# Kernel optimization log

Measured on AMD Instinct MI355X. Metric: run time of the kernel, lower is better.

The kernel has to match this reference:

```python
import jax, jax.numpy as jnp
import numpy as np

B, DM, H, W = 2, 96, 48, 48
E = 192          # d_expand == d_inner
R, N = 6, 16     # delta_rank, d_state


def conv2d(x, w, b, groups=1, pad=0):
    out = jax.lax.conv_general_dilated(
        x, w, window_strides=(1, 1), padding=[(pad, pad), (pad, pad)],
        dimension_numbers=("NCHW", "OIHW", "NCHW"), feature_group_count=groups)
    return out + b[None, :, None, None]


def setup_inputs() -> dict:
    key = jax.random.key(0)
    ks = jax.random.split(key, 24)
    f = lambda k, shape, s: jax.random.normal(k, shape, jnp.float32) * s
    inp = {
        "x": jax.random.normal(ks[0], (B, DM, H, W), jnp.float32),
        "in_proj_w": f(ks[1], (2 * E, DM), 0.05),
        "conv_w": f(ks[2], (E, 1, 3, 3), 0.2),
        "conv_b": f(ks[3], (E,), 0.1),
        "x_proj_w": f(ks[4], (4, R + 2 * N, E), 0.01),
        "dt_proj_w": f(ks[5], (4, E, R), 0.01),
        "dt_proj_b": jnp.full((4, E), -9.0) + f(ks[6], (4, E), 0.1),
        "A_log": jnp.tile(jnp.log(jnp.arange(1, N + 1, dtype=jnp.float32))[None, None, :], (4, E, 1)),
        "Ds": jnp.ones((4, E), jnp.float32),
        "ln_g": jnp.ones(E, jnp.float32), "ln_b": jnp.zeros(E, jnp.float32),
        "c1_w": f(ks[7], (2 * E, E, 1, 1), 0.05), "c1_b": jnp.zeros(2 * E),
        "bn1_g": jnp.ones(2 * E), "bn1_b": jnp.zeros(2 * E), "bn1_m": jnp.zeros(2 * E), "bn1_v": jnp.ones(2 * E),
        "c2_w": f(ks[8], (2 * E, 1, 3, 3), 0.2), "c2_b": jnp.zeros(2 * E),
        "bn2_g": jnp.ones(2 * E), "bn2_b": jnp.zeros(2 * E), "bn2_m": jnp.zeros(2 * E), "bn2_v": jnp.ones(2 * E),
        "c3_w": f(ks[9], (E // 2, 2 * E, 1, 1), 0.05), "c3_b": jnp.zeros(E // 2),
        "se1_w": f(ks[10], (E // 4, E // 2), 0.1), "se1_b": jnp.zeros(E // 4),
        "se2_w": f(ks[11], (E // 2, E // 4), 0.1), "se2_b": jnp.zeros(E // 2),
    }
    return inp


def reference(x, in_proj_w, conv_w, conv_b, x_proj_w, dt_proj_w, dt_proj_b,
              A_log, Ds, ln_g, ln_b,
              c1_w, c1_b, bn1_g, bn1_b, bn1_m, bn1_v,
              c2_w, c2_b, bn2_g, bn2_b, bn2_m, bn2_v,
              c3_w, c3_b, se1_w, se1_b, se2_w, se2_b):
    Bs, _, Hs, Ws = x.shape
    L = Hs * Ws
    # in projection (Linear over channel dim), split x/z gates
    xz = jnp.einsum("bchw,oc->bohw", x, in_proj_w)
    xi, z = jnp.split(xz, 2, axis=1)
    # depthwise conv + SiLU
    xi = jax.nn.silu(conv2d(xi, conv_w, conv_b, groups=E, pad=1))
    # ---- selective scan (4-direction cross scan, cumsum formulation) ----
    xf = xi.reshape(Bs, E, L)
    xt = jnp.swapaxes(xi, 2, 3).reshape(Bs, E, L)
    xs = jnp.stack([xf, xf[..., ::-1], xt, xt[..., ::-1]], axis=1)  # [B,4,E,L]
    dbc = jnp.einsum("bkcl,krc->bkrl", xs, x_proj_w)                # [B,4,R+2N,L]
    dlt, b, c = dbc[:, :, :R], dbc[:, :, R:R + N], dbc[:, :, R + N:]
    dlt = jnp.einsum("bkrl,kdr->bkdl", dlt, dt_proj_w) + dt_proj_b[None, :, :, None]
    dlt = jax.nn.softplus(dlt)                                      # [B,4,E,L]
    dA = dlt[..., None] * A_log[None, :, :, None, :]                # [B,4,E,L,N]
    phi = jnp.exp(-jnp.cumsum(dA, axis=3))
    dbx = dlt[..., None] * jnp.swapaxes(b, 2, 3)[:, :, None] * xs[..., None]  # [B,4,E,L,N]
    h = phi * jnp.cumsum(dbx / (phi + 1e-12), axis=3)
    y = jnp.einsum("bkdln,bknl->bkdl", h, c) + Ds[None, :, :, None]  # [B,4,E,L]
    # ---- cross merge ----
    y1 = y[:, 0]
    y2 = y[:, 1, :, ::-1]
    y3 = jnp.swapaxes(y[:, 2].reshape(Bs, E, Ws, Hs), 2, 3).reshape(Bs, E, L)
    y4 = jnp.swapaxes(y[:, 3, :, ::-1].reshape(Bs, E, Ws, Hs), 2, 3).reshape(Bs, E, L)
    ys = (y1 + y2 + y3 + y4).reshape(Bs, E, Hs, Ws)
    # layernorm over channels
    yn = jnp.moveaxis(ys, 1, -1)
    mu = yn.mean(-1, keepdims=True)
    var = yn.var(-1, keepdims=True)
    yn = (yn - mu) / jnp.sqrt(var + 1e-5) * ln_g + ln_b
    u = jnp.moveaxis(yn, -1, 1) * z
    # ---- EFFN ----
    def bn(t, g, bb, m, v):
        return (t - m[None, :, None, None]) / jnp.sqrt(v + 1e-5)[None, :, None, None] * g[None, :, None, None] + bb[None, :, None, None]
    t = jax.nn.relu(bn(conv2d(u, c1_w, c1_b), bn1_g, bn1_b, bn1_m, bn1_v))
    t = jax.nn.relu(bn(conv2d(t, c2_w, c2_b, groups=2 * E, pad=1), bn2_g, bn2_b, bn2_m, bn2_v))
    t = conv2d(t, c3_w, c3_b)
    # squeeze-excitation: t + t * sigmoid(fc(relu(fc(avgpool(t)))))
    s = t.mean((2, 3))
    s = jax.nn.relu(s @ se1_w.T + se1_b)
    s = jax.nn.sigmoid(s @ se2_w.T + se2_b)
    return t + t * s[:, :, None, None]
```

## Files before the change

kernel.cpp:

```cpp
#include <hip/hip_runtime.h>
#include <hip/hip_bf16.h>

#define LTOT 2304
#define ECH  192
#define NCH  16
#define CCH  96
#define SCH  24

__device__ __forceinline__ int permS(int k, int l) {
  if (k == 0) return l;
  if (k == 1) return LTOT - 1 - l;
  int m = (k == 2) ? l : (LTOT - 1 - l);
  return (m % 48) * 48 + (m / 48);
}

__device__ __forceinline__ float sp_fast(float x) {
  float t = __expf(x);
  return (t <= 0.018f) ? t * fmaf(t, fmaf(t, 0.33333334f, -0.5f), 1.f) : log1pf(t);
}

__global__ __launch_bounds__(256) void k1_inproj(const float* __restrict__ x,
                                                 const float* __restrict__ W,
                                                 float* __restrict__ xi_pre,
                                                 float* __restrict__ z) {
  const int l0 = blockIdx.x * 64;
  const int o0 = blockIdx.y * 64;
  const int b  = blockIdx.z;
  __shared__ __align__(16) float xs[96 * 66];
  __shared__ __align__(16) float Wl[96 * 68];
  const int tid = threadIdx.x;
  for (int idx = tid; idx < 96 * 64; idx += 256) {
    int i = idx & 63, cc = idx >> 6;
    xs[cc * 66 + i] = x[(b * 96 + cc) * LTOT + l0 + i];
  }
  for (int idx = tid; idx < 64 * 96; idx += 256) {
    int r = idx / 96, cc = idx - r * 96;
    Wl[cc * 68 + r] = W[(o0 + r) * 96 + cc];
  }
  __syncthreads();
  const int lane = tid & 63, w = tid >> 6;
  const int jj = lane & 15, rqq = lane >> 4;
  const int rbase = 16 * w + 4 * rqq;
  float acc[4][4];
#pragma unroll
  for (int p = 0; p < 4; ++p)
#pragma unroll
    for (int t = 0; t < 4; ++t) acc[p][t] = 0.f;
#pragma unroll 2
  for (int cc = 0; cc < 96; ++cc) {
    const float4 wv = *(const float4*)&Wl[cc * 68 + rbase];
    const float2 xa = *(const float2*)&xs[cc * 66 + 2 * jj];
    const float2 xb = *(const float2*)&xs[cc * 66 + 32 + 2 * jj];
    acc[0][0] = fmaf(wv.x, xa.x, acc[0][0]); acc[0][1] = fmaf(wv.y, xa.x, acc[0][1]);
    acc[0][2] = fmaf(wv.z, xa.x, acc[0][2]); acc[0][3] = fmaf(wv.w, xa.x, acc[0][3]);
    acc[1][0] = fmaf(wv.x, xa.y, acc[1][0]); acc[1][1] = fmaf(wv.y, xa.y, acc[1][1]);
    acc[1][2] = fmaf(wv.z, xa.y, acc[1][2]); acc[1][3] = fmaf(wv.w, xa.y, acc[1][3]);
    acc[2][0] = fmaf(wv.x, xb.x, acc[2][0]); acc[2][1] = fmaf(wv.y, xb.x, acc[2][1]);
    acc[2][2] = fmaf(wv.z, xb.x, acc[2][2]); acc[2][3] = fmaf(wv.w, xb.x, acc[2][3]);
    acc[3][0] = fmaf(wv.x, xb.y, acc[3][0]); acc[3][1] = fmaf(wv.y, xb.y, acc[3][1]);
    acc[3][2] = fmaf(wv.z, xb.y, acc[3][2]); acc[3][3] = fmaf(wv.w, xb.y, acc[3][3]);
  }
  __syncthreads();
  float* ol = xs;
#pragma unroll
  for (int t = 0; t < 4; ++t) {
    ol[(rbase + t) * 65 + 2 * jj]      = acc[0][t];
    ol[(rbase + t) * 65 + 2 * jj + 1]  = acc[1][t];
    ol[(rbase + t) * 65 + 2 * jj + 32] = acc[2][t];
    ol[(rbase + t) * 65 + 2 * jj + 33] = acc[3][t];
  }
  __syncthreads();
  for (int idx = tid; idx < 64 * 64; idx += 256) {
    int r = idx & 63, pos = idx >> 6;
    float v = ol[r * 65 + pos];
    int o = o0 + r, l = l0 + pos;
    if (o < ECH) xi_pre[(b * LTOT + l) * ECH + o] = v;
    else         z[(b * LTOT + l) * ECH + (o - ECH)] = v;
  }
}

__global__ __launch_bounds__(256) void k2_dwconv(const float* __restrict__ xi_pre,
                                                 const float* __restrict__ cw,
                                                 const float* __restrict__ cb,
                                                 float* __restrict__ xi) {
  int g = blockIdx.x * 256 + threadIdx.x;
  if (g >= 2 * LTOT * ECH) return;
  int e = g % ECH; int l = (g / ECH) % LTOT; int b = g / (ECH * LTOT);
  int h = l / 48, wq = l % 48;
  float acc = cb[e];
#pragma unroll
  for (int kh = 0; kh < 3; ++kh) {
    int hh = h + kh - 1; if (hh < 0 || hh >= 48) continue;
#pragma unroll
    for (int kw = 0; kw < 3; ++kw) {
      int ww = wq + kw - 1; if (ww < 0 || ww >= 48) continue;
      acc = fmaf(cw[e * 9 + kh * 3 + kw], xi_pre[(b * LTOT + hh * 48 + ww) * ECH + e], acc);
    }
  }
  xi[g] = acc / (1.f + __expf(-acc));
}

__global__ __launch_bounds__(256) void k3_xproj(const float* __restrict__ xi,
                                                const float* __restrict__ xw,
                                                float* __restrict__ dl6g,
                                                float* __restrict__ bT,
                                                float* __restrict__ cT) {
  const int l0 = blockIdx.x * 32;
  const int k  = blockIdx.y;
  const int b  = blockIdx.z;
  __shared__ __align__(16) float xs[96 * 34];
  __shared__ __align__(16) float Wl[192 * 40];
  __shared__ float dl6[6 * 33];
  const int tid = threadIdx.x;
  const float* wsrc = xw + k * 38 * ECH;
  for (int idx = tid; idx < 38 * 192; idx += 256) {
    int r = idx / 192, cc = idx - r * 192;
    Wl[cc * 40 + r] = wsrc[idx];
  }
  const int lane = tid & 63, w = tid >> 6;
  const int jj = lane & 15;
  const int rq = w * 4 + (lane >> 4);
  const int rqc = rq < 9 ? rq : 9;
  const int j0 = 2 * jj;
  float a00 = 0.f, a01 = 0.f, a02 = 0.f, a03 = 0.f;
  float a10 = 0.f, a11 = 0.f, a12 = 0.f, a13 = 0.f;
  for (int kc = 0; kc < 2; ++kc) {
    __syncthreads();
    for (int idx = tid; idx < 32 * 96; idx += 256) {
      int j = idx / 96, cc = idx - j * 96;
      int s = permS(k, l0 + j);
      xs[cc * 34 + j] = xi[(b * LTOT + s) * ECH + kc * 96 + cc];
    }
    __syncthreads();
#pragma unroll 4
    for (int cc = 0; cc < 96; ++cc) {
      const float2 xv = *(const float2*)&xs[cc * 34 + j0];
      const float4 wv = *(const float4*)&Wl[(kc * 96 + cc) * 40 + 4 * rqc];
      a00 = fmaf(wv.x, xv.x, a00); a01 = fmaf(wv.y, xv.x, a01);
      a02 = fmaf(wv.z, xv.x, a02); a03 = fmaf(wv.w, xv.x, a03);
      a10 = fmaf(wv.x, xv.y, a10); a11 = fmaf(wv.y, xv.y, a11);
      a12 = fmaf(wv.z, xv.y, a12); a13 = fmaf(wv.w, xv.y, a13);
    }
  }
  const int bk = b * 4 + k;
  if (rq < 10) {
    float av[2][4] = {{a00, a01, a02, a03}, {a10, a11, a12, a13}};
#pragma unroll
    for (int t = 0; t < 4; ++t) {
      int r = 4 * rq + t;
      if (r >= 38) continue;
#pragma unroll
      for (int p = 0; p < 2; ++p) {
        int j = j0 + p;
        float v = av[p][t];
        if (r < 6)       dl6g[((bk * LTOT) + l0 + j) * 6 + r] = v;
        else if (r < 22) bT[((bk * LTOT) + l0 + j) * NCH + (r - 6)] = v;
        else             cT[((bk * LTOT) + l0 + j) * NCH + (r - 22)] = v;
      }
    }
  }
}

__global__ __launch_bounds__(256) void k4a_scan1(const float* __restrict__ dl6g,
                                                 const float* __restrict__ xi,
                                                 const float* __restrict__ bT,
                                                 const float* __restrict__ Alog,
                                                 const float* __restrict__ dtw,
                                                 const float* __restrict__ dtb,
                                                 float* __restrict__ q,
                                                 float* __restrict__ Ts) {
  const int cb = blockIdx.x;
  const int db = blockIdx.y;
  const int bk = blockIdx.z;
  const int b = bk >> 2, k = bk & 3;
  const int l0 = cb * 96;
  __shared__ __align__(16) float2 sdx[48 * 64];
  __shared__ __align__(16) float  sb[96 * NCH];
  __shared__ __align__(16) float  sdl6[96 * 6];
  const int tid = threadIdx.x;
  const int dd = tid & 63, cg = tid >> 6;
  const int dg = db * 64 + dd;
  float b6 = dtb[k * ECH + dg];
  float w6[6];
  {
    const float2* d2 = (const float2*)(dtw + (k * ECH + dg) * 6);
    float2 u0 = d2[0], u1 = d2[1], u2 = d2[2];
    w6[0] = u0.x; w6[1] = u0.y; w6[2] = u1.x; w6[3] = u1.y; w6[4] = u2.x; w6[5] = u2.y;
  }
  for (int idx = tid; idx < 96 * 6; idx += 256) sdl6[idx] = dl6g[(bk * LTOT + l0) * 6 + idx];
  for (int idx = tid; idx < 96 * NCH; idx += 256) sb[idx] = bT[(bk * LTOT + l0) * NCH + idx];
  float C1[16], h[16];
#pragma unroll
  for (int n = 0; n < 16; ++n) {
    C1[n] = Alog[(k * ECH + dg) * NCH + n];
    h[n] = 0.f;
  }
  float Tsum = 0.f;
  const int c = cb * 4 + cg;
  for (int half = 0; half < 2; ++half) {
    __syncthreads();
    for (int e = tid; e < 48 * 64; e += 256) {
      int s = e >> 6;
      int j = (s / 12) * 24 + half * 12 + (s % 12);
      const float* d6 = sdl6 + j * 6;
      float xa = b6;
#pragma unroll
      for (int r = 0; r < 6; ++r) xa = fmaf(w6[r], d6[r], xa);
      float dl = sp_fast(xa);
      int sp = permS(k, l0 + j);
      float xiv = xi[(b * LTOT + sp) * ECH + dg];
      sdx[s * 64 + dd] = make_float2(dl, xiv);
    }
    __syncthreads();
    for (int i = 0; i < 12; ++i) {
      int j = cg * 24 + half * 12 + i;
      float2 dx = sdx[(cg * 12 + i) * 64 + dd];
      float dl = dx.x;
      float u  = dl * dx.y;
      Tsum += dl;
      const float4* bb4 = (const float4*)(sb + j * NCH);
      float4 q0 = bb4[0], q1 = bb4[1], q2 = bb4[2], q3 = bb4[3];
      float bbl[16] = {q0.x, q0.y, q0.z, q0.w, q1.x, q1.y, q1.z, q1.w,
                       q2.x, q2.y, q2.z, q2.w, q3.x, q3.y, q3.z, q3.w};
      if (dl <= 0.018f) {
#pragma unroll
        for (int n = 0; n < 16; ++n) {
          float xn = C1[n] * dl;
          float e = fmaf(xn, fmaf(xn, fmaf(xn, -(1.f / 6.f), 0.5f), -1.f), 1.f);
          h[n] = fmaf(e, h[n], u * bbl[n]);
        }
      } else {
#pragma unroll
        for (int n = 0; n < 16; ++n) {
          float e = __expf(-C1[n] * dl);
          h[n] = fmaf(e, h[n], u * bbl[n]);
        }
      }
    }
  }
  float4* qp = (float4*)(q + ((bk * CCH + c) * ECH + dg) * NCH);
  qp[0] = make_float4(h[0], h[1], h[2], h[3]);
  qp[1] = make_float4(h[4], h[5], h[6], h[7]);
  qp[2] = make_float4(h[8], h[9], h[10], h[11]);
  qp[3] = make_float4(h[12], h[13], h[14], h[15]);
  Ts[(bk * CCH + c) * ECH + dg] = Tsum;
}

__global__ __launch_bounds__(256) void k4b_comb(const float* __restrict__ Alog,
                                                const float* __restrict__ Ts,
                                                float* __restrict__ q) {
  int t = blockIdx.x * 256 + threadIdx.x;
  if (t >= 8 * ECH * NCH) return;
  int n = t & 15, d = (t >> 4) % ECH, bk = t / (NCH * ECH);
  int k = bk & 3;
  float A = Alog[(k * ECH + d) * NCH + n];
  float h = 0.f;
  for (int c = 0; c < CCH; ++c) {
    int base = ((bk * CCH + c) * ECH + d) * NCH + n;
    float qc = q[base];
    q[base] = h;
    float xv = A * Ts[(bk * CCH + c) * ECH + d];
    float P = (xv <= 0.05f)
                  ? fmaf(xv, fmaf(xv, fmaf(xv, -(1.f / 6.f), 0.5f), -1.f), 1.f)
                  : __expf(-xv);
    h = fmaf(P, h, qc);
  }
}

__global__ __launch_bounds__(256) void k4c_scan2(const float* __restrict__ dl6g,
                                                 const float* __restrict__ xi,
                                                 const float* __restrict__ bT,
                                                 const float* __restrict__ cT,
                                                 const float* __restrict__ Alog,
                                                 const float* __restrict__ dtw,
                                                 const float* __restrict__ dtb,
                                                 const float* __restrict__ hin,
                                                 float* __restrict__ yd) {
  const int cb = blockIdx.x;
  const int db = blockIdx.y;
  const int bk = blockIdx.z;
  const int b = bk >> 2, k = bk & 3;
  const int l0 = cb * 96;
  __shared__ __align__(16) float2 sdx[48 * 64];
  __shared__ __align__(16) float  sb[96 * NCH];
  __shared__ __align__(16) float  sc[96 * NCH];
  __shared__ __align__(16) float  sdl6[96 * 6];
  const int tid = threadIdx.x;
  const int dd = tid & 63, cg = tid >> 6;
  const int dg = db * 64 + dd;
  float b6 = dtb[k * ECH + dg];
  float w6[6];
  {
    const float2* d2 = (const float2*)(dtw + (k * ECH + dg) * 6);
    float2 u0 = d2[0], u1 = d2[1], u2 = d2[2];
    w6[0] = u0.x; w6[1] = u0.y; w6[2] = u1.x; w6[3] = u1.y; w6[4] = u2.x; w6[5] = u2.y;
  }
  for (int idx = tid; idx < 96 * 6; idx += 256) sdl6[idx] = dl6g[(bk * LTOT + l0) * 6 + idx];
  for (int idx = tid; idx < 96 * NCH; idx += 256) {
    sb[idx] = bT[(bk * LTOT + l0) * NCH + idx];
    sc[idx] = cT[(bk * LTOT + l0) * NCH + idx];
  }
  float C1[16], h[16];
  const int c = cb * 4 + cg;
  const float4* hp = (const float4*)(hin + ((bk * CCH + c) * ECH + dg) * NCH);
  {
    float4 h0 = hp[0], h1 = hp[1], h2 = hp[2], h3 = hp[3];
    h[0]=h0.x; h[1]=h0.y; h[2]=h0.z; h[3]=h0.w;
    h[4]=h1.x; h[5]=h1.y; h[6]=h1.z; h[7]=h1.w;
    h[8]=h2.x; h[9]=h2.y; h[10]=h2.z; h[11]=h2.w;
    h[12]=h3.x; h[13]=h3.y; h[14]=h3.z; h[15]=h3.w;
  }
#pragma unroll
  for (int n = 0; n < 16; ++n) C1[n] = Alog[(k * ECH + dg) * NCH + n];
  float* ydk = yd + (b * 4 + k) * LTOT * ECH;
  for (int half = 0; half < 2; ++half) {
    __syncthreads();
    for (int e = tid; e < 48 * 64; e += 256) {
      int s = e >> 6;
      int j = (s / 12) * 24 + half * 12 + (s % 12);
      const float* d6 = sdl6 + j * 6;
      float xa = b6;
#pragma unroll
      for (int r = 0; r < 6; ++r) xa = fmaf(w6[r], d6[r], xa);
      float dl = sp_fast(xa);
      int sp = permS(k, l0 + j);
      float xiv = xi[(b * LTOT + sp) * ECH + dg];
      sdx[s * 64 + dd] = make_float2(dl, xiv);
    }
    __syncthreads();
    for (int i = 0; i < 12; ++i) {
      int j = cg * 24 + half * 12 + i;
      float2 dx = sdx[(cg * 12 + i) * 64 + dd];
      float dl = dx.x;
      float u  = dl * dx.y;
      const float4* bb4 = (const float4*)(sb + j * NCH);
      float4 q0 = bb4[0], q1 = bb4[1], q2 = bb4[2], q3 = bb4[3];
      float bbl[16] = {q0.x, q0.y, q0.z, q0.w, q1.x, q1.y, q1.z, q1.w,
                       q2.x, q2.y, q2.z, q2.w, q3.x, q3.y, q3.z, q3.w};
      if (dl <= 0.018f) {
#pragma unroll
        for (int n = 0; n < 16; ++n) {
          float xn = C1[n] * dl;
          float e = fmaf(xn, fmaf(xn, fmaf(xn, -(1.f / 6.f), 0.5f), -1.f), 1.f);
          h[n] = fmaf(e, h[n], u * bbl[n]);
        }
      } else {
#pragma unroll
        for (int n = 0; n < 16; ++n) {
          float e = __expf(-C1[n] * dl);
          h[n] = fmaf(e, h[n], u * bbl[n]);
        }
      }
      const float4* cc4 = (const float4*)(sc + j * NCH);
      float4 c0 = cc4[0], c1 = cc4[1], c2 = cc4[2], c3 = cc4[3];
      float ccl[16] = {c0.x, c0.y, c0.z, c0.w, c1.x, c1.y, c1.z, c1.w,
                       c2.x, c2.y, c2.z, c2.w, c3.x, c3.y, c3.z, c3.w};
      float y = 0.f;
#pragma unroll
      for (int n = 0; n < 16; ++n) y = fmaf(h[n], ccl[n], y);
      int sp = permS(k, l0 + j);
      ydk[sp * ECH + dg] = y;
    }
  }
}

__global__ __launch_bounds__(256) void k5_ln(const float* __restrict__ yd,
                                             const float* __restrict__ Ds,
                                             const float* __restrict__ lng,
                                             const float* __restrict__ lnb,
                                             float* __restrict__ zu) {
  int p = blockIdx.x * 4 + (threadIdx.x >> 6);
  int lane = threadIdx.x & 63;
  int b = (p >= LTOT) ? 1 : 0;
  int l = p - b * LTOT;
  const float* y0 = yd + (b * 4) * LTOT * ECH + l * ECH;
  float vd[3], sd[3];
#pragma unroll
  for (int t = 0; t < 3; ++t) {
    int d = lane + t * 64;
    vd[t] = ((y0[d] + y0[LTOT * ECH + d]) + y0[2 * LTOT * ECH + d]) + y0[3 * LTOT * ECH + d];
    sd[t] = Ds[d] + Ds[ECH + d] + Ds[2 * ECH + d] + Ds[3 * ECH + d];
  }
  float s1 = vd[0] + vd[1] + vd[2];
  float s2 = sd[0] + sd[1] + sd[2];
#pragma unroll
  for (int off = 32; off > 0; off >>= 1) {
    s1 += __shfl_xor(s1, off, 64);
    s2 += __shfl_xor(s2, off, 64);
  }
  float mean_dot = s1 * (1.f / 192.f);
  float mean_sd  = s2 * (1.f / 192.f);
  float dev[3];
  float ss = 0.f;
#pragma unroll
  for (int t = 0; t < 3; ++t) {
    dev[t] = (vd[t] - mean_dot) + (sd[t] - mean_sd);
    ss = fmaf(dev[t], dev[t], ss);
  }
#pragma unroll
  for (int off = 32; off > 0; off >>= 1) ss += __shfl_xor(ss, off, 64);
  float rstd = 1.f / sqrtf(ss * (1.f / 192.f) + 1e-5f);
#pragma unroll
  for (int t = 0; t < 3; ++t) {
    int d = lane + t * 64;
    float yn = (dev[t] * rstd) * lng[d] + lnb[d];
    zu[p * ECH + d] = yn * zu[p * ECH + d];
  }
}

__global__ __launch_bounds__(256) void k6_c1(const float* __restrict__ u,
                                             const float* __restrict__ W,
                                             const float* __restrict__ c1b,
                                             const float* __restrict__ g1,
                                             const float* __restrict__ b1,
                                             const float* __restrict__ m1,
                                             const float* __restrict__ v1,
                                             float* __restrict__ t1,
                                             float* __restrict__ se) {
  const int l0 = blockIdx.x * 64;
  const int o0 = blockIdx.y * 64;
  const int b  = blockIdx.z;
  const int tid = threadIdx.x;
  if (blockIdx.x == 0 && blockIdx.y == 0 && blockIdx.z == 0 && tid < 192) se[tid] = 0.f;
  __shared__ __align__(16) float xs[96 * 66];
  __shared__ __align__(16) float Wl[96 * 68];
  const int lane = tid & 63, w = tid >> 6;
  const int jj = lane & 15, rqq = lane >> 4;
  const int rbase = 16 * w + 4 * rqq;
  float acc[4][4];
#pragma unroll
  for (int p = 0; p < 4; ++p)
#pragma unroll
    for (int t = 0; t < 4; ++t) acc[p][t] = 0.f;
  for (int kc = 0; kc < 2; ++kc) {
    if (kc) __syncthreads();
    for (int idx = tid; idx < 64 * 96; idx += 256) {
      int i = idx / 96, cc = idx - i * 96;
      xs[cc * 66 + i] = u[(b * LTOT + l0 + i) * ECH + kc * 96 + cc];
    }
    for (int idx = tid; idx < 64 * 96; idx += 256) {
      int r = idx / 96, cc = idx - r * 96;
      Wl[cc * 68 + r] = W[(o0 + r) * ECH + kc * 96 + cc];
    }
    __syncthreads();
#pragma unroll 2
    for (int cc = 0; cc < 96; ++cc) {
      const float4 wv = *(const float4*)&Wl[cc * 68 + rbase];
      const float2 xa = *(const float2*)&xs[cc * 66 + 2 * jj];
      const float2 xb = *(const float2*)&xs[cc * 66 + 32 + 2 * jj];
      acc[0][0] = fmaf(wv.x, xa.x, acc[0][0]); acc[0][1] = fmaf(wv.y, xa.x, acc[0][1]);
      acc[0][2] = fmaf(wv.z, xa.x, acc[0][2]); acc[0][3] = fmaf(wv.w, xa.x, acc[0][3]);
      acc[1][0] = fmaf(wv.x, xa.y, acc[1][0]); acc[1][1] = fmaf(wv.y, xa.y, acc[1][1]);
      acc[1][2] = fmaf(wv.z, xa.y, acc[1][2]); acc[1][3] = fmaf(wv.w, xa.y, acc[1][3]);
      acc[2][0] = fmaf(wv.x, xb.x, acc[2][0]); acc[2][1] = fmaf(wv.y, xb.x, acc[2][1]);
      acc[2][2] = fmaf(wv.z, xb.x, acc[2][2]); acc[2][3] = fmaf(wv.w, xb.x, acc[2][3]);
      acc[3][0] = fmaf(wv.x, xb.y, acc[3][0]); acc[3][1] = fmaf(wv.y, xb.y, acc[3][1]);
      acc[3][2] = fmaf(wv.z, xb.y, acc[3][2]); acc[3][3] = fmaf(wv.w, xb.y, acc[3][3]);
    }
  }
#pragma unroll
  for (int t = 0; t < 4; ++t) {
    int o = o0 + rbase + t;
    float sc = g1[o] / sqrtf(v1[o] + 1e-5f);
    float bias = (c1b[o] - m1[o]) * sc + b1[o];
#pragma unroll
    for (int p = 0; p < 4; ++p) acc[p][t] = fmaxf(fmaf(acc[p][t], sc, bias), 0.f);
  }
  __syncthreads();
  float* ol = xs;
#pragma unroll
  for (int t = 0; t < 4; ++t) {
    ol[(rbase + t) * 65 + 2 * jj]      = acc[0][t];
    ol[(rbase + t) * 65 + 2 * jj + 1]  = acc[1][t];
    ol[(rbase + t) * 65 + 2 * jj + 32] = acc[2][t];
    ol[(rbase + t) * 65 + 2 * jj + 33] = acc[3][t];
  }
  __syncthreads();
  for (int idx = tid; idx < 64 * 64; idx += 256) {
    int pos = idx & 63, r = idx >> 6;
    t1[(b * 384 + o0 + r) * LTOT + l0 + pos] = ol[r * 65 + pos];
  }
}

__global__ __launch_bounds__(256) void k7_dw2(const float* __restrict__ t1,
                                              const float* __restrict__ cw,
                                              const float* __restrict__ cb,
                                              const float* __restrict__ g2,
                                              const float* __restrict__ b2,
                                              const float* __restrict__ m2,
                                              const float* __restrict__ v2,
                                              float* __restrict__ t2) {
  int g = blockIdx.x * 256 + threadIdx.x;
  if (g >= 2 * LTOT * 384) return;
  int l = g % LTOT; int o = (g / LTOT) % 384; int b = g / (LTOT * 384);
  int h = l / 48, wq = l % 48;
  const float* src = t1 + (b * 384 + o) * LTOT;
  float acc = cb[o];
#pragma unroll
  for (int kh = 0; kh < 3; ++kh) {
    int hh = h + kh - 1; if (hh < 0 || hh >= 48) continue;
#pragma unroll
    for (int kw = 0; kw < 3; ++kw) {
      int ww = wq + kw - 1; if (ww < 0 || ww >= 48) continue;
      acc = fmaf(cw[o * 9 + kh * 3 + kw], src[hh * 48 + ww], acc);
    }
  }
  float sc = g2[o] / sqrtf(v2[o] + 1e-5f);
  float val = (acc - m2[o]) * sc + b2[o];
  t2[g] = fmaxf(val, 0.f);
}

__global__ __launch_bounds__(256) void k8_c3(const float* __restrict__ t2,
                                             const float* __restrict__ W,
                                             const float* __restrict__ c3b,
                                             float* __restrict__ t3,
                                             float* __restrict__ se) {
  const int l0 = blockIdx.x * 32;
  const int r0 = blockIdx.y * 32;
  const int b  = blockIdx.z;
  __shared__ __align__(16) float Wl[384 * 34];
  __shared__ __align__(16) float xs[192 * 34];
  const int tid = threadIdx.x;
  const int lane = tid & 63, w = tid >> 6;
  const int jj = lane & 15, rqq = lane >> 4;
  const int rloc = 8 * w + 2 * rqq;
  for (int idx = tid; idx < 32 * 384; idx += 256) {
    int r = idx / 384, cc = idx - r * 384;
    Wl[cc * 34 + r] = W[(r0 + r) * 384 + cc];
  }
  float acc[2][2];
  acc[0][0] = acc[0][1] = acc[1][0] = acc[1][1] = 0.f;
  for (int kc = 0; kc < 2; ++kc) {
    if (kc) __syncthreads();
    for (int idx = tid; idx < 192 * 32; idx += 256) {
      int i = idx & 31, cc = idx >> 5;
      xs[cc * 34 + i] = t2[(b * 384 + kc * 192 + cc) * LTOT + l0 + i];
    }
    __syncthreads();
#pragma unroll 4
    for (int cc = 0; cc < 192; ++cc) {
      const float2 wv = *(const float2*)&Wl[(kc * 192 + cc) * 34 + rloc];
      const float2 xv = *(const float2*)&xs[cc * 34 + 2 * jj];
      acc[0][0] = fmaf(wv.x, xv.x, acc[0][0]); acc[0][1] = fmaf(wv.y, xv.x, acc[0][1]);
      acc[1][0] = fmaf(wv.x, xv.y, acc[1][0]); acc[1][1] = fmaf(wv.y, xv.y, acc[1][1]);
    }
  }
  {
    float b0 = c3b[r0 + rloc], b1v = c3b[r0 + rloc + 1];
    acc[0][0] += b0; acc[1][0] += b0; acc[0][1] += b1v; acc[1][1] += b1v;
  }
#pragma unroll
  for (int t = 0; t < 2; ++t) {
    float v = acc[0][t] + acc[1][t];
    v += __shfl_xor(v, 1); v += __shfl_xor(v, 2);
    v += __shfl_xor(v, 4); v += __shfl_xor(v, 8);
    if (jj == 0) atomicAdd(&se[b * 96 + r0 + rloc + t], v);
  }
  __syncthreads();
  float* ol = xs;
#pragma unroll
  for (int t = 0; t < 2; ++t) {
    ol[(rloc + t) * 33 + 2 * jj]     = acc[0][t];
    ol[(rloc + t) * 33 + 2 * jj + 1] = acc[1][t];
  }
  __syncthreads();
  for (int idx = tid; idx < 32 * 32; idx += 256) {
    int pos = idx & 31, r = idx >> 5;
    t3[(b * 96 + r0 + r) * LTOT + l0 + pos] = ol[r * 33 + pos];
  }
}

__global__ __launch_bounds__(256) void k9a_se(const float* __restrict__ se,
                                              const float* __restrict__ w1,
                                              const float* __restrict__ sb1,
                                              const float* __restrict__ w2,
                                              const float* __restrict__ sb2,
                                              float* __restrict__ smul) {
  __shared__ float sm[192];
  __shared__ float s1[96];
  int t = threadIdx.x;
  if (t < 192) sm[t] = se[t] * (1.f / 2304.f);
  __syncthreads();
  if (t < 96) {
    int b = t / 48, i = t % 48;
    float acc = sb1[i];
    for (int m = 0; m < 96; ++m) acc = fmaf(w1[i * 96 + m], sm[b * 96 + m], acc);
    s1[t] = fmaxf(acc, 0.f);
  }
  __syncthreads();
  if (t < 192) {
    int b = t / 96, j = t % 96;
    float acc = sb2[j];
    for (int i = 0; i < 48; ++i) acc = fmaf(w2[j * 48 + i], s1[b * 48 + i], acc);
    smul[t] = 1.f + 1.f / (1.f + __expf(-acc));
  }
}

__global__ __launch_bounds__(256) void k9b_out(const float* __restrict__ t3,
                                               const float* __restrict__ smul,
                                               float* __restrict__ out) {
  int g = blockIdx.x * 256 + threadIdx.x;
  if (g >= 2 * 96 * LTOT) return;
  int bj = g / LTOT;
  out[g] = t3[g] * smul[bj];
}

extern "C" void kernel_launch(void* const* d_in, const int* in_sizes, int n_in,
                              void* d_out, int out_size, void* d_ws, size_t ws_size,
                              hipStream_t stream) {
  const float* x     = (const float*)d_in[0];
  const float* inw   = (const float*)d_in[1];
  const float* convw = (const float*)d_in[2];
  const float* convb = (const float*)d_in[3];
  const float* xpw   = (const float*)d_in[4];
  const float* dtw   = (const float*)d_in[5];
  const float* dtb   = (const float*)d_in[6];
  const float* Alog  = (const float*)d_in[7];
  const float* Ds    = (const float*)d_in[8];
  const float* lng   = (const float*)d_in[9];
  const float* lnb   = (const float*)d_in[10];
  const float* c1w   = (const float*)d_in[11];
  const float* c1b   = (const float*)d_in[12];
  const float* bn1g  = (const float*)d_in[13];
  const float* bn1b  = (const float*)d_in[14];
  const float* bn1m  = (const float*)d_in[15];
  const float* bn1v  = (const float*)d_in[16];
  const float* c2w   = (const float*)d_in[17];
  const float* c2b   = (const float*)d_in[18];
  const float* bn2g  = (const float*)d_in[19];
  const float* bn2b  = (const float*)d_in[20];
  const float* bn2m  = (const float*)d_in[21];
  const float* bn2v  = (const float*)d_in[22];
  const float* c3w   = (const float*)d_in[23];
  const float* c3b   = (const float*)d_in[24];
  const float* se1w  = (const float*)d_in[25];
  const float* se1b  = (const float*)d_in[26];
  const float* se2w  = (const float*)d_in[27];
  const float* se2b  = (const float*)d_in[28];

  float* ws = (float*)d_ws;
  float* xi_pre = ws;
  float* z      = ws + 884736;
  float* xi     = ws + 1769472;
  float* dl6g   = ws + 2654208;
  float* bT     = ws + 2764800;
  float* cT     = ws + 3354624;
  float* q      = ws + 3944448;
  float* Ts     = ws + 6303744;
  float* se     = ws + 6451200;
  float* smul   = ws + 6451392;
  float* yd     = ws + 6451584;
  float* t1 = yd;
  float* t2 = yd + 1769472;
  float* t3 = q;

  k1_inproj<<<dim3(36, 6, 2), 256, 0, stream>>>(x, inw, xi_pre, z);
  k2_dwconv<<<3456, 256, 0, stream>>>(xi_pre, convw, convb, xi);
  k3_xproj<<<dim3(72, 4, 2), 256, 0, stream>>>(xi, xpw, dl6g, bT, cT);
  k4a_scan1<<<dim3(24, 3, 8), 256, 0, stream>>>(dl6g, xi, bT, Alog, dtw, dtb, q, Ts);
  k4b_comb<<<96, 256, 0, stream>>>(Alog, Ts, q);
  k4c_scan2<<<dim3(24, 3, 8), 256, 0, stream>>>(dl6g, xi, bT, cT, Alog, dtw, dtb, q, yd);
  k5_ln<<<1152, 256, 0, stream>>>(yd, Ds, lng, lnb, z);
  k6_c1<<<dim3(36, 6, 2), 256, 0, stream>>>(z, c1w, c1b, bn1g, bn1b, bn1m, bn1v, t1, se);
  k7_dw2<<<6912, 256, 0, stream>>>(t1, c2w, c2b, bn2g, bn2b, bn2m, bn2v, t2);
  k8_c3<<<dim3(72, 3, 2), 256, 0, stream>>>(t2, c3w, c3b, t3, se);
  k9a_se<<<1, 256, 0, stream>>>(se, se1w, se1b, se2w, se2b, smul);
  k9b_out<<<1728, 256, 0, stream>>>(t3, smul, (float*)d_out);
}
```

Baseline: 317.5 us.

## Halve tile sizes, double scan chunks, fuse SE into output kernel

The in-projection and first EFFN conv now use 32-position tiles instead of 64, doubling their grids. The chunked scan uses 192 chunks of 12 steps instead of 96 of 24, so the scan kernels run 48x3x8 blocks that each load all 48 positions in one pass with no half loop. The q and Ts workspace grows to match. The separate single-block SE kernel is folded into the output kernel, so every block recomputes the tiny SE MLP redundantly. These changes aim for more parallelism and fewer launches, at the cost of more combine work in k4b, larger q traffic and duplicated SE arithmetic.

```diff
diff --git a/kernel.cpp b/kernel.cpp
--- a/kernel.cpp
+++ b/kernel.cpp
@@ -4,8 +4,8 @@
 #define LTOT 2304
 #define ECH  192
 #define NCH  16
-#define CCH  96
-#define SCH  24
+#define CCH  192
+#define SCH  12
 
 __device__ __forceinline__ int permS(int k, int l) {
   if (k == 0) return l;
@@ -23,15 +23,15 @@
                                                  const float* __restrict__ W,
                                                  float* __restrict__ xi_pre,
                                                  float* __restrict__ z) {
-  const int l0 = blockIdx.x * 64;
+  const int l0 = blockIdx.x * 32;
   const int o0 = blockIdx.y * 64;
   const int b  = blockIdx.z;
-  __shared__ __align__(16) float xs[96 * 66];
+  __shared__ __align__(16) float xs[96 * 34];
   __shared__ __align__(16) float Wl[96 * 68];
   const int tid = threadIdx.x;
-  for (int idx = tid; idx < 96 * 64; idx += 256) {
-    int i = idx & 63, cc = idx >> 6;
-    xs[cc * 66 + i] = x[(b * 96 + cc) * LTOT + l0 + i];
+  for (int idx = tid; idx < 96 * 32; idx += 256) {
+    int i = idx & 31, cc = idx >> 5;
+    xs[cc * 34 + i] = x[(b * 96 + cc) * LTOT + l0 + i];
   }
   for (int idx = tid; idx < 64 * 96; idx += 256) {
     int r = idx / 96, cc = idx - r * 96;
@@ -41,38 +41,31 @@
   const int lane = tid & 63, w = tid >> 6;
   const int jj = lane & 15, rqq = lane >> 4;
   const int rbase = 16 * w + 4 * rqq;
-  float acc[4][4];
-#pragma unroll
-  for (int p = 0; p < 4; ++p)
+  float acc[2][4];
+#pragma unroll
+  for (int p = 0; p < 2; ++p)
 #pragma unroll
     for (int t = 0; t < 4; ++t) acc[p][t] = 0.f;
-#pragma unroll 2
+#pragma unroll 4
   for (int cc = 0; cc < 96; ++cc) {
     const float4 wv = *(const float4*)&Wl[cc * 68 + rbase];
-    const float2 xa = *(const float2*)&xs[cc * 66 + 2 * jj];
-    const float2 xb = *(const float2*)&xs[cc * 66 + 32 + 2 * jj];
-    acc[0][0] = fmaf(wv.x, xa.x, acc[0][0]); acc[0][1] = fmaf(wv.y, xa.x, acc[0][1]);
-    acc[0][2] = fmaf(wv.z, xa.x, acc[0][2]); acc[0][3] = fmaf(wv.w, xa.x, acc[0][3]);
-    acc[1][0] = fmaf(wv.x, xa.y, acc[1][0]); acc[1][1] = fmaf(wv.y, xa.y, acc[1][1]);
-    acc[1][2] = fmaf(wv.z, xa.y, acc[1][2]); acc[1][3] = fmaf(wv.w, xa.y, acc[1][3]);
-    acc[2][0] = fmaf(wv.x, xb.x, acc[2][0]); acc[2][1] = fmaf(wv.y, xb.x, acc[2][1]);
-    acc[2][2] = fmaf(wv.z, xb.x, acc[2][2]); acc[2][3] = fmaf(wv.w, xb.x, acc[2][3]);
-    acc[3][0] = fmaf(wv.x, xb.y, acc[3][0]); acc[3][1] = fmaf(wv.y, xb.y, acc[3][1]);
-    acc[3][2] = fmaf(wv.z, xb.y, acc[3][2]); acc[3][3] = fmaf(wv.w, xb.y, acc[3][3]);
+    const float2 xv = *(const float2*)&xs[cc * 34 + 2 * jj];
+    acc[0][0] = fmaf(wv.x, xv.x, acc[0][0]); acc[0][1] = fmaf(wv.y, xv.x, acc[0][1]);
+    acc[0][2] = fmaf(wv.z, xv.x, acc[0][2]); acc[0][3] = fmaf(wv.w, xv.x, acc[0][3]);
+    acc[1][0] = fmaf(wv.x, xv.y, acc[1][0]); acc[1][1] = fmaf(wv.y, xv.y, acc[1][1]);
+    acc[1][2] = fmaf(wv.z, xv.y, acc[1][2]); acc[1][3] = fmaf(wv.w, xv.y, acc[1][3]);
   }
   __syncthreads();
   float* ol = xs;
 #pragma unroll
   for (int t = 0; t < 4; ++t) {
-    ol[(rbase + t) * 65 + 2 * jj]      = acc[0][t];
-    ol[(rbase + t) * 65 + 2 * jj + 1]  = acc[1][t];
-    ol[(rbase + t) * 65 + 2 * jj + 32] = acc[2][t];
-    ol[(rbase + t) * 65 + 2 * jj + 33] = acc[3][t];
-  }
-  __syncthreads();
-  for (int idx = tid; idx < 64 * 64; idx += 256) {
+    ol[(rbase + t) * 33 + 2 * jj]     = acc[0][t];
+    ol[(rbase + t) * 33 + 2 * jj + 1] = acc[1][t];
+  }
+  __syncthreads();
+  for (int idx = tid; idx < 32 * 64; idx += 256) {
     int r = idx & 63, pos = idx >> 6;
-    float v = ol[r * 65 + pos];
+    float v = ol[r * 33 + pos];
     int o = o0 + r, l = l0 + pos;
     if (o < ECH) xi_pre[(b * LTOT + l) * ECH + o] = v;
     else         z[(b * LTOT + l) * ECH + (o - ECH)] = v;
@@ -110,7 +103,6 @@
   const int b  = blockIdx.z;
   __shared__ __align__(16) float xs[96 * 34];
   __shared__ __align__(16) float Wl[192 * 40];
-  __shared__ float dl6[6 * 33];
   const int tid = threadIdx.x;
   const float* wsrc = xw + k * 38 * ECH;
   for (int idx = tid; idx < 38 * 192; idx += 256) {
@@ -173,10 +165,9 @@
   const int db = blockIdx.y;
   const int bk = blockIdx.z;
   const int b = bk >> 2, k = bk & 3;
-  const int l0 = cb * 96;
+  const int l0 = cb * 48;
   __shared__ __align__(16) float2 sdx[48 * 64];
-  __shared__ __align__(16) float  sb[96 * NCH];
-  __shared__ __align__(16) float  sdl6[96 * 6];
+  __shared__ __align__(16) float  sb[48 * NCH];
   const int tid = threadIdx.x;
   const int dd = tid & 63, cg = tid >> 6;
   const int dg = db * 64 + dd;
@@ -187,57 +178,51 @@
     float2 u0 = d2[0], u1 = d2[1], u2 = d2[2];
     w6[0] = u0.x; w6[1] = u0.y; w6[2] = u1.x; w6[3] = u1.y; w6[4] = u2.x; w6[5] = u2.y;
   }
-  for (int idx = tid; idx < 96 * 6; idx += 256) sdl6[idx] = dl6g[(bk * LTOT + l0) * 6 + idx];
-  for (int idx = tid; idx < 96 * NCH; idx += 256) sb[idx] = bT[(bk * LTOT + l0) * NCH + idx];
+  for (int idx = tid; idx < 48 * NCH; idx += 256) sb[idx] = bT[(bk * LTOT + l0) * NCH + idx];
+  for (int e = tid; e < 48 * 64; e += 256) {
+    int s = e >> 6;
+    const float* d6 = dl6g + (bk * LTOT + l0 + s) * 6;
+    float xa = b6;
+#pragma unroll
+    for (int r = 0; r < 6; ++r) xa = fmaf(w6[r], d6[r], xa);
+    float dl = sp_fast(xa);
+    int sp = permS(k, l0 + s);
+    sdx[s * 64 + dd] = make_float2(dl, xi[(b * LTOT + sp) * ECH + dg]);
+  }
   float C1[16], h[16];
 #pragma unroll
   for (int n = 0; n < 16; ++n) {
     C1[n] = Alog[(k * ECH + dg) * NCH + n];
     h[n] = 0.f;
   }
+  __syncthreads();
   float Tsum = 0.f;
+  for (int i = 0; i < SCH; ++i) {
+    int j = cg * SCH + i;
+    float2 dx = sdx[j * 64 + dd];
+    float dl = dx.x;
+    float u  = dl * dx.y;
+    Tsum += dl;
+    const float4* bb4 = (const float4*)(sb + j * NCH);
+    float4 q0 = bb4[0], q1 = bb4[1], q2 = bb4[2], q3 = bb4[3];
+    float bbl[16] = {q0.x, q0.y, q0.z, q0.w, q1.x, q1.y, q1.z, q1.w,
+                     q2.x, q2.y, q2.z, q2.w, q3.x, q3.y, q3.z, q3.w};
+    if (dl <= 0.018f) {
+#pragma unroll
+      for (int n = 0; n < 16; ++n) {
+        float xn = C1[n] * dl;
+        float e = fmaf(xn, fmaf(xn, fmaf(xn, -(1.f / 6.f), 0.5f), -1.f), 1.f);
+        h[n] = fmaf(e, h[n], u * bbl[n]);
+      }
+    } else {
+#pragma unroll
+      for (int n = 0; n < 16; ++n) {
+        float e = __expf(-C1[n] * dl);
+        h[n] = fmaf(e, h[n], u * bbl[n]);
+      }
+    }
+  }
   const int c = cb * 4 + cg;
-  for (int half = 0; half < 2; ++half) {
-    __syncthreads();
-    for (int e = tid; e < 48 * 64; e += 256) {
-      int s = e >> 6;
-      int j = (s / 12) * 24 + half * 12 + (s % 12);
-      const float* d6 = sdl6 + j * 6;
-      float xa = b6;
-#pragma unroll
-      for (int r = 0; r < 6; ++r) xa = fmaf(w6[r], d6[r], xa);
-      float dl = sp_fast(xa);
-      int sp = permS(k, l0 + j);
-      float xiv = xi[(b * LTOT + sp) * ECH + dg];
-      sdx[s * 64 + dd] = make_float2(dl, xiv);
-    }
-    __syncthreads();
-    for (int i = 0; i < 12; ++i) {
-      int j = cg * 24 + half * 12 + i;
-      float2 dx = sdx[(cg * 12 + i) * 64 + dd];
-      float dl = dx.x;
-      float u  = dl * dx.y;
-      Tsum += dl;
-      const float4* bb4 = (const float4*)(sb + j * NCH);
-      float4 q0 = bb4[0], q1 = bb4[1], q2 = bb4[2], q3 = bb4[3];
-      float bbl[16] = {q0.x, q0.y, q0.z, q0.w, q1.x, q1.y, q1.z, q1.w,
-                       q2.x, q2.y, q2.z, q2.w, q3.x, q3.y, q3.z, q3.w};
-      if (dl <= 0.018f) {
-#pragma unroll
-        for (int n = 0; n < 16; ++n) {
-          float xn = C1[n] * dl;
-          float e = fmaf(xn, fmaf(xn, fmaf(xn, -(1.f / 6.f), 0.5f), -1.f), 1.f);
-          h[n] = fmaf(e, h[n], u * bbl[n]);
-        }
-      } else {
-#pragma unroll
-        for (int n = 0; n < 16; ++n) {
-          float e = __expf(-C1[n] * dl);
-          h[n] = fmaf(e, h[n], u * bbl[n]);
-        }
-      }
-    }
-  }
   float4* qp = (float4*)(q + ((bk * CCH + c) * ECH + dg) * NCH);
   qp[0] = make_float4(h[0], h[1], h[2], h[3]);
   qp[1] = make_float4(h[4], h[5], h[6], h[7]);
@@ -255,6 +240,7 @@
   int k = bk & 3;
   float A = Alog[(k * ECH + d) * NCH + n];
   float h = 0.f;
+#pragma unroll 4
   for (int c = 0; c < CCH; ++c) {
     int base = ((bk * CCH + c) * ECH + d) * NCH + n;
     float qc = q[base];
@@ -280,11 +266,10 @@
   const int db = blockIdx.y;
   const int bk = blockIdx.z;
   const int b = bk >> 2, k = bk & 3;
-  const int l0 = cb * 96;
+  const int l0 = cb * 48;
   __shared__ __align__(16) float2 sdx[48 * 64];
-  __shared__ __align__(16) float  sb[96 * NCH];
-  __shared__ __align__(16) float  sc[96 * NCH];
-  __shared__ __align__(16) float  sdl6[96 * 6];
+  __shared__ __align__(16) float  sb[48 * NCH];
+  __shared__ __align__(16) float  sc[48 * NCH];
   const int tid = threadIdx.x;
   const int dd = tid & 63, cg = tid >> 6;
   const int dg = db * 64 + dd;
@@ -295,10 +280,19 @@
     float2 u0 = d2[0], u1 = d2[1], u2 = d2[2];
     w6[0] = u0.x; w6[1] = u0.y; w6[2] = u1.x; w6[3] = u1.y; w6[4] = u2.x; w6[5] = u2.y;
   }
-  for (int idx = tid; idx < 96 * 6; idx += 256) sdl6[idx] = dl6g[(bk * LTOT + l0) * 6 + idx];
-  for (int idx = tid; idx < 96 * NCH; idx += 256) {
+  for (int idx = tid; idx < 48 * NCH; idx += 256) {
     sb[idx] = bT[(bk * LTOT + l0) * NCH + idx];
     sc[idx] = cT[(bk * LTOT + l0) * NCH + idx];
+  }
+  for (int e = tid; e < 48 * 64; e += 256) {
+    int s = e >> 6;
+    const float* d6 = dl6g + (bk * LTOT + l0 + s) * 6;
+    float xa = b6;
+#pragma unroll
+    for (int r = 0; r < 6; ++r) xa = fmaf(w6[r], d6[r], xa);
+    float dl = sp_fast(xa);
+    int sp = permS(k, l0 + s);
+    sdx[s * 64 + dd] = make_float2(dl, xi[(b * LTOT + sp) * ECH + dg]);
   }
   float C1[16], h[16];
   const int c = cb * 4 + cg;
@@ -313,54 +307,39 @@
 #pragma unroll
   for (int n = 0; n < 16; ++n) C1[n] = Alog[(k * ECH + dg) * NCH + n];
   float* ydk = yd + (b * 4 + k) * LTOT * ECH;
-  for (int half = 0; half < 2; ++half) {
-    __syncthreads();
-    for (int e = tid; e < 48 * 64; e += 256) {
-      int s = e >> 6;
-      int j = (s / 12) * 24 + half * 12 + (s % 12);
-      const float* d6 = sdl6 + j * 6;
-      float xa = b6;
-#pragma unroll
-      for (int r = 0; r < 6; ++r) xa = fmaf(w6[r], d6[r], xa);
-      float dl = sp_fast(xa);
-      int sp = permS(k, l0 + j);
-      float xiv = xi[(b * LTOT + sp) * ECH + dg];
-      sdx[s * 64 + dd] = make_float2(dl, xiv);
-    }
-    __syncthreads();
-    for (int i = 0; i < 12; ++i) {
-      int j = cg * 24 + half * 12 + i;
-      float2 dx = sdx[(cg * 12 + i) * 64 + dd];
-      float dl = dx.x;
-      float u  = dl * dx.y;
-      const float4* bb4 = (const float4*)(sb + j * NCH);
-      float4 q0 = bb4[0], q1 = bb4[1], q2 = bb4[2], q3 = bb4[3];
-      float bbl[16] = {q0.x, q0.y, q0.z, q0.w, q1.x, q1.y, q1.z, q1.w,
-                       q2.x, q2.y, q2.z, q2.w, q3.x, q3.y, q3.z, q3.w};
-      if (dl <= 0.018f) {
-#pragma unroll
-        for (int n = 0; n < 16; ++n) {
-          float xn = C1[n] * dl;
-          float e = fmaf(xn, fmaf(xn, fmaf(xn, -(1.f / 6.f), 0.5f), -1.f), 1.f);
-          h[n] = fmaf(e, h[n], u * bbl[n]);
-        }
-      } else {
-#pragma unroll
-        for (int n = 0; n < 16; ++n) {
-          float e = __expf(-C1[n] * dl);
-          h[n] = fmaf(e, h[n], u * bbl[n]);
-        }
+  __syncthreads();
+  for (int i = 0; i < SCH; ++i) {
+    int j = cg * SCH + i;
+    float2 dx = sdx[j * 64 + dd];
+    float dl = dx.x;
+    float u  = dl * dx.y;
+    const float4* bb4 = (const float4*)(sb + j * NCH);
+    float4 q0 = bb4[0], q1 = bb4[1], q2 = bb4[2], q3 = bb4[3];
+    float bbl[16] = {q0.x, q0.y, q0.z, q0.w, q1.x, q1.y, q1.z, q1.w,
+                     q2.x, q2.y, q2.z, q2.w, q3.x, q3.y, q3.z, q3.w};
+    if (dl <= 0.018f) {
+#pragma unroll
+      for (int n = 0; n < 16; ++n) {
+        float xn = C1[n] * dl;
+        float e = fmaf(xn, fmaf(xn, fmaf(xn, -(1.f / 6.f), 0.5f), -1.f), 1.f);
+        h[n] = fmaf(e, h[n], u * bbl[n]);
       }
-      const float4* cc4 = (const float4*)(sc + j * NCH);
-      float4 c0 = cc4[0], c1 = cc4[1], c2 = cc4[2], c3 = cc4[3];
-      float ccl[16] = {c0.x, c0.y, c0.z, c0.w, c1.x, c1.y, c1.z, c1.w,
-                       c2.x, c2.y, c2.z, c2.w, c3.x, c3.y, c3.z, c3.w};
-      float y = 0.f;
-#pragma unroll
-      for (int n = 0; n < 16; ++n) y = fmaf(h[n], ccl[n], y);
-      int sp = permS(k, l0 + j);
-      ydk[sp * ECH + dg] = y;
-    }
+    } else {
+#pragma unroll
+      for (int n = 0; n < 16; ++n) {
+        float e = __expf(-C1[n] * dl);
+        h[n] = fmaf(e, h[n], u * bbl[n]);
+      }
+    }
+    const float4* cc4 = (const float4*)(sc + j * NCH);
+    float4 c0 = cc4[0], c1 = cc4[1], c2 = cc4[2], c3 = cc4[3];
+    float ccl[16] = {c0.x, c0.y, c0.z, c0.w, c1.x, c1.y, c1.z, c1.w,
+                     c2.x, c2.y, c2.z, c2.w, c3.x, c3.y, c3.z, c3.w};
+    float y = 0.f;
+#pragma unroll
+    for (int n = 0; n < 16; ++n) y = fmaf(h[n], ccl[n], y);
+    int sp = permS(k, l0 + j);
+    ydk[sp * ECH + dg] = y;
   }
 }
 
@@ -417,45 +396,40 @@
                                              const float* __restrict__ v1,
                                              float* __restrict__ t1,
                                              float* __restrict__ se) {
-  const int l0 = blockIdx.x * 64;
+  const int l0 = blockIdx.x * 32;
   const int o0 = blockIdx.y * 64;
   const int b  = blockIdx.z;
   const int tid = threadIdx.x;
   if (blockIdx.x == 0 && blockIdx.y == 0 && blockIdx.z == 0 && tid < 192) se[tid] = 0.f;
-  __shared__ __align__(16) float xs[96 * 66];
+  __shared__ __align__(16) float xs[96 * 34];
   __shared__ __align__(16) float Wl[96 * 68];
   const int lane = tid & 63, w = tid >> 6;
   const int jj = lane & 15, rqq = lane >> 4;
   const int rbase = 16 * w + 4 * rqq;
-  float acc[4][4];
-#pragma unroll
-  for (int p = 0; p < 4; ++p)
+  float acc[2][4];
+#pragma unroll
+  for (int p = 0; p < 2; ++p)
 #pragma unroll
     for (int t = 0; t < 4; ++t) acc[p][t] = 0.f;
   for (int kc = 0; kc < 2; ++kc) {
     if (kc) __syncthreads();
-    for (int idx = tid; idx < 64 * 96; idx += 256) {
-      int i = idx / 96, cc = idx - i * 96;
-      xs[cc * 66 + i] = u[(b * LTOT + l0 + i) * ECH + kc * 96 + cc];
+    for (int idx = tid; idx < 32 * 96; idx += 256) {
+      int cc = idx % 96, i = idx / 96;
+      xs[cc * 34 + i] = u[(b * LTOT + l0 + i) * ECH + kc * 96 + cc];
     }
     for (int idx = tid; idx < 64 * 96; idx += 256) {
       int r = idx / 96, cc = idx - r * 96;
       Wl[cc * 68 + r] = W[(o0 + r) * ECH + kc * 96 + cc];
     }
     __syncthreads();
-#pragma unroll 2
+#pragma unroll 4
     for (int cc = 0; cc < 96; ++cc) {
       const float4 wv = *(const float4*)&Wl[cc * 68 + rbase];
-      const float2 xa = *(const float2*)&xs[cc * 66 + 2 * jj];
-      const float2 xb = *(const float2*)&xs[cc * 66 + 32 + 2 * jj];
-      acc[0][0] = fmaf(wv.x, xa.x, acc[0][0]); acc[0][1] = fmaf(wv.y, xa.x, acc[0][1]);
-      acc[0][2] = fmaf(wv.z, xa.x, acc[0][2]); acc[0][3] = fmaf(wv.w, xa.x, acc[0][3]);
-      acc[1][0] = fmaf(wv.x, xa.y, acc[1][0]); acc[1][1] = fmaf(wv.y, xa.y, acc[1][1]);
-      acc[1][2] = fmaf(wv.z, xa.y, acc[1][2]); acc[1][3] = fmaf(wv.w, xa.y, acc[1][3]);
-      acc[2][0] = fmaf(wv.x, xb.x, acc[2][0]); acc[2][1] = fmaf(wv.y, xb.x, acc[2][1]);
-      acc[2][2] = fmaf(wv.z, xb.x, acc[2][2]); acc[2][3] = fmaf(wv.w, xb.x, acc[2][3]);
-      acc[3][0] = fmaf(wv.x, xb.y, acc[3][0]); acc[3][1] = fmaf(wv.y, xb.y, acc[3][1]);
-      acc[3][2] = fmaf(wv.z, xb.y, acc[3][2]); acc[3][3] = fmaf(wv.w, xb.y, acc[3][3]);
+      const float2 xv = *(const float2*)&xs[cc * 34 + 2 * jj];
+      acc[0][0] = fmaf(wv.x, xv.x, acc[0][0]); acc[0][1] = fmaf(wv.y, xv.x, acc[0][1]);
+      acc[0][2] = fmaf(wv.z, xv.x, acc[0][2]); acc[0][3] = fmaf(wv.w, xv.x, acc[0][3]);
+      acc[1][0] = fmaf(wv.x, xv.y, acc[1][0]); acc[1][1] = fmaf(wv.y, xv.y, acc[1][1]);
+      acc[1][2] = fmaf(wv.z, xv.y, acc[1][2]); acc[1][3] = fmaf(wv.w, xv.y, acc[1][3]);
     }
   }
 #pragma unroll
@@ -464,21 +438,19 @@
     float sc = g1[o] / sqrtf(v1[o] + 1e-5f);
     float bias = (c1b[o] - m1[o]) * sc + b1[o];
 #pragma unroll
-    for (int p = 0; p < 4; ++p) acc[p][t] = fmaxf(fmaf(acc[p][t], sc, bias), 0.f);
+    for (int p = 0; p < 2; ++p) acc[p][t] = fmaxf(fmaf(acc[p][t], sc, bias), 0.f);
   }
   __syncthreads();
   float* ol = xs;
 #pragma unroll
   for (int t = 0; t < 4; ++t) {
-    ol[(rbase + t) * 65 + 2 * jj]      = acc[0][t];
-    ol[(rbase + t) * 65 + 2 * jj + 1]  = acc[1][t];
-    ol[(rbase + t) * 65 + 2 * jj + 32] = acc[2][t];
-    ol[(rbase + t) * 65 + 2 * jj + 33] = acc[3][t];
-  }
-  __syncthreads();
-  for (int idx = tid; idx < 64 * 64; idx += 256) {
-    int pos = idx & 63, r = idx >> 6;
-    t1[(b * 384 + o0 + r) * LTOT + l0 + pos] = ol[r * 65 + pos];
+    ol[(rbase + t) * 33 + 2 * jj]     = acc[0][t];
+    ol[(rbase + t) * 33 + 2 * jj + 1] = acc[1][t];
+  }
+  __syncthreads();
+  for (int idx = tid; idx < 32 * 64; idx += 256) {
+    int pos = idx & 31, r = idx >> 5;
+    t1[(b * 384 + o0 + r) * LTOT + l0 + pos] = ol[r * 33 + pos];
   }
 }
 
@@ -570,39 +542,37 @@
   }
 }
 
-__global__ __launch_bounds__(256) void k9a_se(const float* __restrict__ se,
+__global__ __launch_bounds__(256) void k9_out(const float* __restrict__ t3,
+                                              const float* __restrict__ se,
                                               const float* __restrict__ w1,
                                               const float* __restrict__ sb1,
                                               const float* __restrict__ w2,
                                               const float* __restrict__ sb2,
-                                              float* __restrict__ smul) {
+                                              float* __restrict__ out) {
   __shared__ float sm[192];
   __shared__ float s1[96];
+  __shared__ float smul[192];
   int t = threadIdx.x;
   if (t < 192) sm[t] = se[t] * (1.f / 2304.f);
   __syncthreads();
   if (t < 96) {
     int b = t / 48, i = t % 48;
-    float acc = sb1[i];
-    for (int m = 0; m < 96; ++m) acc = fmaf(w1[i * 96 + m], sm[b * 96 + m], acc);
-    s1[t] = fmaxf(acc, 0.f);
+    float a = sb1[i];
+#pragma unroll 4
+    for (int m = 0; m < 96; ++m) a = fmaf(w1[i * 96 + m], sm[b * 96 + m], a);
+    s1[t] = fmaxf(a, 0.f);
   }
   __syncthreads();
   if (t < 192) {
     int b = t / 96, j = t % 96;
-    float acc = sb2[j];
-    for (int i = 0; i < 48; ++i) acc = fmaf(w2[j * 48 + i], s1[b * 48 + i], acc);
-    smul[t] = 1.f + 1.f / (1.f + __expf(-acc));
-  }
-}
-
-__global__ __launch_bounds__(256) void k9b_out(const float* __restrict__ t3,
-                                               const float* __restrict__ smul,
-                                               float* __restrict__ out) {
-  int g = blockIdx.x * 256 + threadIdx.x;
-  if (g >= 2 * 96 * LTOT) return;
-  int bj = g / LTOT;
-  out[g] = t3[g] * smul[bj];
+    float a = sb2[j];
+#pragma unroll 4
+    for (int i = 0; i < 48; ++i) a = fmaf(w2[j * 48 + i], s1[b * 48 + i], a);
+    smul[t] = 1.f + 1.f / (1.f + __expf(-a));
+  }
+  __syncthreads();
+  int g = blockIdx.x * 256 + t;
+  if (g < 2 * 96 * LTOT) out[g] = t3[g] * smul[g / LTOT];
 }
 
 extern "C" void kernel_launch(void* const* d_in, const int* in_sizes, int n_in,
@@ -646,24 +616,22 @@
   float* bT     = ws + 2764800;
   float* cT     = ws + 3354624;
   float* q      = ws + 3944448;
-  float* Ts     = ws + 6303744;
-  float* se     = ws + 6451200;
-  float* smul   = ws + 6451392;
-  float* yd     = ws + 6451584;
+  float* Ts     = ws + 13381632;
+  float* se     = ws + 13676544;
+  float* yd     = ws + 13676736;
   float* t1 = yd;
   float* t2 = yd + 1769472;
   float* t3 = q;
 
-  k1_inproj<<<dim3(36, 6, 2), 256, 0, stream>>>(x, inw, xi_pre, z);
+  k1_inproj<<<dim3(72, 6, 2), 256, 0, stream>>>(x, inw, xi_pre, z);
   k2_dwconv<<<3456, 256, 0, stream>>>(xi_pre, convw, convb, xi);
   k3_xproj<<<dim3(72, 4, 2), 256, 0, stream>>>(xi, xpw, dl6g, bT, cT);
-  k4a_scan1<<<dim3(24, 3, 8), 256, 0, stream>>>(dl6g, xi, bT, Alog, dtw, dtb, q, Ts);
+  k4a_scan1<<<dim3(48, 3, 8), 256, 0, stream>>>(dl6g, xi, bT, Alog, dtw, dtb, q, Ts);
   k4b_comb<<<96, 256, 0, stream>>>(Alog, Ts, q);
-  k4c_scan2<<<dim3(24, 3, 8), 256, 0, stream>>>(dl6g, xi, bT, cT, Alog, dtw, dtb, q, yd);
+  k4c_scan2<<<dim3(48, 3, 8), 256, 0, stream>>>(dl6g, xi, bT, cT, Alog, dtw, dtb, q, yd);
   k5_ln<<<1152, 256, 0, stream>>>(yd, Ds, lng, lnb, z);
-  k6_c1<<<dim3(36, 6, 2), 256, 0, stream>>>(z, c1w, c1b, bn1g, bn1b, bn1m, bn1v, t1, se);
+  k6_c1<<<dim3(72, 6, 2), 256, 0, stream>>>(z, c1w, c1b, bn1g, bn1b, bn1m, bn1v, t1, se);
   k7_dw2<<<6912, 256, 0, stream>>>(t1, c2w, c2b, bn2g, bn2b, bn2m, bn2v, t2);
   k8_c3<<<dim3(72, 3, 2), 256, 0, stream>>>(t2, c3w, c3b, t3, se);
-  k9a_se<<<1, 256, 0, stream>>>(se, se1w, se1b, se2w, se2b, smul);
-  k9b_out<<<1728, 256, 0, stream>>>(t3, smul, (float*)d_out);
-}
+  k9_out<<<1728, 256, 0, stream>>>(t3, se, se1w, se1b, se2w, se2b, (float*)d_out);
+}
```

New measurement: 341.6 us. 7.6% more time.
